# Kernel optimization log

Hardware: AMD Instinct MI355X
Metric: run time of the kernel (lower is better)

The kernel has to match this reference:

```python
import jax, jax.numpy as jnp
import numpy as np

D_MODEL = 4096
N_EXPERTS = 64
TOP_K = 2
EPS = 1e-8


def setup_inputs() -> dict:
    key = jax.random.key(0)
    k1, k2, k3, k4 = jax.random.split(key, 4)
    hidden_states = jax.random.normal(k1, (4, 4096, D_MODEL), dtype=jnp.float32)
    routing_bias = jax.random.normal(k2, (4, N_EXPERTS), dtype=jnp.float32)
    # nn.Linear(d_model, n_experts): weight [n_experts, d_model], bias [n_experts]
    bound = 1.0 / np.sqrt(D_MODEL)
    W = jax.random.uniform(k3, (N_EXPERTS, D_MODEL), dtype=jnp.float32, minval=-bound, maxval=bound)
    b = jax.random.uniform(k4, (N_EXPERTS,), dtype=jnp.float32, minval=-bound, maxval=bound)
    return {"hidden_states": hidden_states, "routing_bias": routing_bias, "W": W, "b": b}


def reference(hidden_states, routing_bias, W, b):
    # router logits: [B, S, E]
    logits = jnp.einsum("bsd,ed->bse", hidden_states, W) + b
    logits = logits + routing_bias[:, None, :]
    expert_weights = jax.nn.softmax(logits, axis=-1)
    top_k_weights, top_k_indices = jax.lax.top_k(expert_weights, TOP_K)
    top_k_weights = top_k_weights / (jnp.sum(top_k_weights, axis=-1, keepdims=True) + EPS)
    return top_k_weights, top_k_indices
```

## Files before the change

### kernel.cpp

```cpp
#include <hip/hip_runtime.h>


#define D          4096
#define NE         64
#define TPB        64
#define KC         32
#define NCHUNK     (D / KC)
#define HP         36
#define LP         65

__global__ __launch_bounds__(256)
void router_kernel(const float* __restrict__ hidden,
                   const float* __restrict__ rbias,
                   const float* __restrict__ W,
                   const float* __restrict__ bias,
                   float* __restrict__ out)
{
    __shared__ __align__(16) float Hs[2][TPB][HP];
    __shared__ __align__(16) float Ws[2][NE][HP];
    __shared__ float Ls[NE * LP];
    __shared__ float Bs[NE];

    const int t   = threadIdx.x;
    const int gt0 = blockIdx.x * TPB;
    const int batch = gt0 >> 12;

    if (t < NE) Bs[t] = bias[t] + rbias[batch * NE + t];

    const int row = t >> 2;
    const int kq4 = (t & 3) << 2;
    const float* hrow = hidden + (size_t)(gt0 + row) * D + kq4;
    const float* wrow = W      + (size_t)row * D + kq4;

    const int l  = t & 63;
    const int w  = t >> 6;
    const int tq = l & 15;
    const int eq = l >> 4;
    const int ebase = w * 16 + eq * 4;

    float acc[4][4] = {};

    float4 ha = *(const float4*)(hrow);
    float4 hb = *(const float4*)(hrow + 16);
    float4 wa = *(const float4*)(wrow);
    float4 wb = *(const float4*)(wrow + 16);
    *(float4*)&Hs[0][row][kq4]      = ha;
    *(float4*)&Hs[0][row][kq4 + 16] = hb;
    *(float4*)&Ws[0][row][kq4]      = wa;
    *(float4*)&Ws[0][row][kq4 + 16] = wb;
    __syncthreads();

    for (int c = 0; c < NCHUNK; ++c) {
        const int buf = c & 1;
        if (c + 1 < NCHUNK) {
            const int k0 = (c + 1) * KC;
            ha = *(const float4*)(hrow + k0);
            hb = *(const float4*)(hrow + k0 + 16);
            wa = *(const float4*)(wrow + k0);
            wb = *(const float4*)(wrow + k0 + 16);
        }
        #pragma unroll
        for (int kq = 0; kq < KC / 4; ++kq) {
            float4 hv[4], wv[4];
            #pragma unroll
            for (int i = 0; i < 4; ++i)
                hv[i] = *(const float4*)&Hs[buf][tq + 16 * i][kq * 4];
            #pragma unroll
            for (int j = 0; j < 4; ++j)
                wv[j] = *(const float4*)&Ws[buf][ebase + j][kq * 4];
            #pragma unroll
            for (int i = 0; i < 4; ++i)
                #pragma unroll
                for (int j = 0; j < 4; ++j) {
                    acc[i][j] += hv[i].x * wv[j].x;
                    acc[i][j] += hv[i].y * wv[j].y;
                    acc[i][j] += hv[i].z * wv[j].z;
                    acc[i][j] += hv[i].w * wv[j].w;
                }
        }
        __syncthreads();
        if (c + 1 < NCHUNK) {
            const int nb = buf ^ 1;
            *(float4*)&Hs[nb][row][kq4]      = ha;
            *(float4*)&Hs[nb][row][kq4 + 16] = hb;
            *(float4*)&Ws[nb][row][kq4]      = wa;
            *(float4*)&Ws[nb][row][kq4 + 16] = wb;
        }
        __syncthreads();
    }

    #pragma unroll
    for (int i = 0; i < 4; ++i)
        #pragma unroll
        for (int j = 0; j < 4; ++j)
            Ls[(ebase + j) * LP + tq + 16 * i] = acc[i][j];
    __syncthreads();

    if (t < TPB) {
        const int tok = t;
        float m = -INFINITY, Z = 0.f;
        float v1 = -INFINITY, v2 = -INFINITY;
        int   i1 = 0, i2 = 0;
        for (int e = 0; e < NE; ++e) {
            const float v = Ls[e * LP + tok] + Bs[e];
            const float nm = fmaxf(m, v);
            Z = Z * __expf(m - nm) + __expf(v - nm);
            m = nm;
            const bool g1 = v > v1;
            const bool g2 = v > v2;
            const float nv2 = g1 ? v1 : (g2 ? v : v2);
            const int   ni2 = g1 ? i1 : (g2 ? e : i2);
            v1 = g1 ? v : v1;
            i1 = g1 ? e : i1;
            v2 = nv2;
            i2 = ni2;
        }
        const float p1 = __expf(v1 - m) / Z;
        const float p2 = __expf(v2 - m) / Z;
        const float s  = p1 + p2 + 1e-8f;
        const int gt = gt0 + tok;
        out[gt * 2 + 0] = p1 / s;
        out[gt * 2 + 1] = p2 / s;
        float* outI = out + 4 * 4096 * 2;
        outI[gt * 2 + 0] = (float)i1;
        outI[gt * 2 + 1] = (float)i2;
    }
}

extern "C" void kernel_launch(void* const* d_in, const int* in_sizes, int n_in,
                              void* d_out, int out_size, void* d_ws, size_t ws_size,
                              hipStream_t stream) {
    (void)in_sizes; (void)n_in; (void)d_ws; (void)ws_size; (void)out_size;
    const float* hidden = (const float*)d_in[0];
    const float* rbias  = (const float*)d_in[1];
    const float* W      = (const float*)d_in[2];
    const float* bias   = (const float*)d_in[3];
    float* out = (float*)d_out;

    const int n_tokens = 4 * 4096;
    dim3 grid(n_tokens / TPB);
    dim3 block(256);
    hipLaunchKernelGGL(router_kernel, grid, block, 0, stream,
                       hidden, rbias, W, bias, out);
}
```

Baseline: 498.3 us.

## Stream hidden tile via global_load_lds and read W directly into registers

Replaces the register-staged shared-memory copy of the hidden tile with asynchronous global-to-LDS loads in a transposed float4 layout. W is no longer staged in shared memory; each wave owns 8 experts and reads their wave-uniform rows straight from global into registers with a one-step prefetch. The block grows to 512 threads, KC to 64, and one of the two barriers per chunk is dropped. This cuts LDS traffic and sync overhead but relies on cache hits for the per-iteration W loads and drops the 4x4 register tiling reuse.

```diff
diff --git a/kernel.cpp b/kernel.cpp
--- a/kernel.cpp
+++ b/kernel.cpp
@@ -1,108 +1,91 @@
 #include <hip/hip_runtime.h>
+#include <stdint.h>
 
 
-#define D          4096
-#define NE         64
-#define TPB        64
-#define KC         32
-#define NCHUNK     (D / KC)
-#define HP         36
-#define LP         65
+#define D     4096
+#define NE    64
+#define TPB   64
+#define KC    64
+#define NCH   (D / KC)
+#define NWAVE 8
+#define EPW   (NE / NWAVE)
 
-__global__ __launch_bounds__(256)
+typedef const __attribute__((address_space(1))) unsigned int* gp_t;
+typedef __attribute__((address_space(3))) unsigned int* lp_t;
+
+__global__ __launch_bounds__(512)
 void router_kernel(const float* __restrict__ hidden,
                    const float* __restrict__ rbias,
                    const float* __restrict__ W,
                    const float* __restrict__ bias,
                    float* __restrict__ out)
 {
-    __shared__ __align__(16) float Hs[2][TPB][HP];
-    __shared__ __align__(16) float Ws[2][NE][HP];
-    __shared__ float Ls[NE * LP];
-    __shared__ float Bs[NE];
+    __shared__ __align__(16) float4 Hs[2][KC / 4][TPB];
+    __shared__ float Ls[NE][TPB];
 
-    const int t   = threadIdx.x;
-    const int gt0 = blockIdx.x * TPB;
+    const int tid   = threadIdx.x;
+    const int lane  = tid & 63;
+    const int w     = __builtin_amdgcn_readfirstlane(tid >> 6);
+    const int gt0   = blockIdx.x * TPB;
     const int batch = gt0 >> 12;
 
-    if (t < NE) Bs[t] = bias[t] + rbias[batch * NE + t];
+    const float* hrow = hidden + (size_t)(gt0 + lane) * D;
+    const float* wb   = W + (size_t)(w * EPW) * D;
 
-    const int row = t >> 2;
-    const int kq4 = (t & 3) << 2;
-    const float* hrow = hidden + (size_t)(gt0 + row) * D + kq4;
-    const float* wrow = W      + (size_t)row * D + kq4;
+    float acc[EPW] = {0.f, 0.f, 0.f, 0.f, 0.f, 0.f, 0.f, 0.f};
 
-    const int l  = t & 63;
-    const int w  = t >> 6;
-    const int tq = l & 15;
-    const int eq = l >> 4;
-    const int ebase = w * 16 + eq * 4;
+    __builtin_amdgcn_global_load_lds((gp_t)(const void*)(hrow + (2 * w) * 4),
+                                     (lp_t)(void*)&Hs[0][2 * w][0], 16, 0, 0);
+    __builtin_amdgcn_global_load_lds((gp_t)(const void*)(hrow + (2 * w + 1) * 4),
+                                     (lp_t)(void*)&Hs[0][2 * w + 1][0], 16, 0, 0);
 
-    float acc[4][4] = {};
+    float4 wc[EPW], wn[EPW];
+    #pragma unroll
+    for (int j = 0; j < EPW; ++j) wc[j] = *(const float4*)(wb + (size_t)j * D);
 
-    float4 ha = *(const float4*)(hrow);
-    float4 hb = *(const float4*)(hrow + 16);
-    float4 wa = *(const float4*)(wrow);
-    float4 wb = *(const float4*)(wrow + 16);
-    *(float4*)&Hs[0][row][kq4]      = ha;
-    *(float4*)&Hs[0][row][kq4 + 16] = hb;
-    *(float4*)&Ws[0][row][kq4]      = wa;
-    *(float4*)&Ws[0][row][kq4 + 16] = wb;
     __syncthreads();
 
-    for (int c = 0; c < NCHUNK; ++c) {
+    for (int c = 0; c < NCH; ++c) {
         const int buf = c & 1;
-        if (c + 1 < NCHUNK) {
-            const int k0 = (c + 1) * KC;
-            ha = *(const float4*)(hrow + k0);
-            hb = *(const float4*)(hrow + k0 + 16);
-            wa = *(const float4*)(wrow + k0);
-            wb = *(const float4*)(wrow + k0 + 16);
+        if (c + 1 < NCH) {
+            const float* src = hrow + (c + 1) * KC;
+            __builtin_amdgcn_global_load_lds((gp_t)(const void*)(src + (2 * w) * 4),
+                                             (lp_t)(void*)&Hs[buf ^ 1][2 * w][0], 16, 0, 0);
+            __builtin_amdgcn_global_load_lds((gp_t)(const void*)(src + (2 * w + 1) * 4),
+                                             (lp_t)(void*)&Hs[buf ^ 1][2 * w + 1][0], 16, 0, 0);
         }
         #pragma unroll
-        for (int kq = 0; kq < KC / 4; ++kq) {
-            float4 hv[4], wv[4];
+        for (int q = 0; q < KC / 4; ++q) {
+            const int k  = c * KC + q * 4;
+            const int kn = (k + 4 < D) ? (k + 4) : 0;
             #pragma unroll
-            for (int i = 0; i < 4; ++i)
-                hv[i] = *(const float4*)&Hs[buf][tq + 16 * i][kq * 4];
+            for (int j = 0; j < EPW; ++j)
+                wn[j] = *(const float4*)(wb + (size_t)j * D + kn);
+            const float4 h = Hs[buf][q][lane];
             #pragma unroll
-            for (int j = 0; j < 4; ++j)
-                wv[j] = *(const float4*)&Ws[buf][ebase + j][kq * 4];
+            for (int j = 0; j < EPW; ++j) {
+                acc[j] += h.x * wc[j].x;
+                acc[j] += h.y * wc[j].y;
+                acc[j] += h.z * wc[j].z;
+                acc[j] += h.w * wc[j].w;
+            }
             #pragma unroll
-            for (int i = 0; i < 4; ++i)
-                #pragma unroll
-                for (int j = 0; j < 4; ++j) {
-                    acc[i][j] += hv[i].x * wv[j].x;
-                    acc[i][j] += hv[i].y * wv[j].y;
-                    acc[i][j] += hv[i].z * wv[j].z;
-                    acc[i][j] += hv[i].w * wv[j].w;
-                }
-        }
-        __syncthreads();
-        if (c + 1 < NCHUNK) {
-            const int nb = buf ^ 1;
-            *(float4*)&Hs[nb][row][kq4]      = ha;
-            *(float4*)&Hs[nb][row][kq4 + 16] = hb;
-            *(float4*)&Ws[nb][row][kq4]      = wa;
-            *(float4*)&Ws[nb][row][kq4 + 16] = wb;
+            for (int j = 0; j < EPW; ++j) wc[j] = wn[j];
         }
         __syncthreads();
     }
 
     #pragma unroll
-    for (int i = 0; i < 4; ++i)
-        #pragma unroll
-        for (int j = 0; j < 4; ++j)
-            Ls[(ebase + j) * LP + tq + 16 * i] = acc[i][j];
+    for (int j = 0; j < EPW; ++j) Ls[w * EPW + j][lane] = acc[j];
     __syncthreads();
 
-    if (t < TPB) {
-        const int tok = t;
+    if (tid < TPB) {
+        const int tok = tid;
         float m = -INFINITY, Z = 0.f;
         float v1 = -INFINITY, v2 = -INFINITY;
         int   i1 = 0, i2 = 0;
         for (int e = 0; e < NE; ++e) {
-            const float v = Ls[e * LP + tok] + Bs[e];
+            const float v = Ls[e][tok] + bias[e] + rbias[batch * NE + e];
             const float nm = fmaxf(m, v);
             Z = Z * __expf(m - nm) + __expf(v - nm);
             m = nm;
@@ -139,7 +122,7 @@
 
     const int n_tokens = 4 * 4096;
     dim3 grid(n_tokens / TPB);
-    dim3 block(256);
+    dim3 block(512);
     hipLaunchKernelGGL(router_kernel, grid, block, 0, stream,
                        hidden, rbias, W, bias, out);
 }
```

Measured after the change: 751.2 us. 1.51x slower.
